# Performance work log

Measured on AMD Instinct MI355X. Metric: run time of the kernel, lower is better.

The kernel has to match this reference:

```python
import jax, jax.numpy as jnp
import numpy as np

N_NODES = 100000
N_EDGES = 200000
Z_DIM = 64
ATTR_DIM = 768
HID = 128
N_CLASSES = 5


def setup_inputs() -> dict:
    key = jax.random.key(0)
    ks = jax.random.split(key, 6)
    z = jax.random.normal(ks[0], (N_NODES, Z_DIM), dtype=jnp.float32)
    edge_index = jax.random.randint(ks[1], (2, N_EDGES), 0, N_NODES, dtype=jnp.int64)
    edge_attr = jax.random.normal(ks[2], (N_EDGES, ATTR_DIM), dtype=jnp.float32)
    W1 = jax.random.normal(ks[3], (ATTR_DIM + Z_DIM, HID), dtype=jnp.float32) * 0.02
    b1 = jnp.zeros((HID,), dtype=jnp.float32)
    W2 = jax.random.normal(ks[4], (HID, N_CLASSES), dtype=jnp.float32) * 0.02
    b2 = jnp.zeros((N_CLASSES,), dtype=jnp.float32)
    return {"z": z, "edge_index": edge_index, "edge_attr": edge_attr,
            "W1": W1, "b1": b1, "W2": W2, "b2": b2}


def reference(z, edge_index, edge_attr, W1, b1, W2, b2):
    # decode(): gather endpoint embeddings, elementwise product  [E, 64]
    node_rep = z[edge_index[0]] * z[edge_index[1]]
    # concat with edge attributes -> [E, 64 + 768] (torch cat order: node_rep first)
    joint = jnp.concatenate([node_rep, edge_attr], axis=-1)
    # 2-layer MLP + softmax
    h = jax.nn.relu(joint @ W1 + b1)
    logits = h @ W2 + b2
    return jax.nn.softmax(logits, axis=-1)
```

## Files before the change

kernel.cpp:

```cpp
#include <hip/hip_runtime.h>
#include <hip/hip_bf16.h>

#define E_TOT 200000
#define NZ 64
#define ATTR_D 768
#define HID_D 128
#define NCLS 5

typedef __attribute__((ext_vector_type(8))) short short8;
typedef __attribute__((ext_vector_type(4))) float f32x4;

typedef __attribute__((address_space(3))) unsigned       lds_u32_t;
typedef const __attribute__((address_space(1))) unsigned glob_u32_t;

__device__ __forceinline__ unsigned pk2(float a, float b) {
    __hip_bfloat162 h = __float22bfloat162_rn(make_float2(a, b));
    return *reinterpret_cast<unsigned*>(&h);
}

__device__ __forceinline__ short8 pack8(const float4 x0, const float4 x1) {
    union { unsigned u[4]; short8 s; } r;
    r.u[0] = pk2(x0.x, x0.y);
    r.u[1] = pk2(x0.z, x0.w);
    r.u[2] = pk2(x1.x, x1.y);
    r.u[3] = pk2(x1.z, x1.w);
    return r.s;
}

__global__ void prep_w1f(const float* __restrict__ W1, __hip_bfloat16* __restrict__ w1f) {
    int idx = blockIdx.x * 256 + threadIdx.x;
    if (idx >= 26 * 8 * 64 * 8) return;
    int j    = idx & 7;
    int lane = (idx >> 3) & 63;
    int f    = (idx >> 9) & 7;
    int kt   = idx >> 12;
    int n = f * 16 + (lane & 15);
    int k = kt * 32 + (lane >> 4) * 8 + j;
    w1f[idx] = __float2bfloat16(W1[(size_t)k * HID_D + n]);
}

__global__ __launch_bounds__(256, 2) void gcn_main(
    const float* __restrict__ z, const int* __restrict__ ei,
    const float* __restrict__ attr, const __hip_bfloat16* __restrict__ w1f,
    const float* __restrict__ b1, const float* __restrict__ W2,
    const float* __restrict__ b2, float* __restrict__ out) {

    __shared__ float As[4][4096];

    const int t    = threadIdx.x;
    const int wv   = t >> 6;
    const int lane = t & 63;
    const int g    = lane >> 4;
    const int c0   = lane & 15;
    const int e0   = blockIdx.x * 128;

    const float* sbase[4];
#pragma unroll
    for (int i = 0; i < 4; ++i) {
        int rsl = i * 8 + (lane >> 3);
        int cch = (lane & 7) ^ (rsl & 7);
        int er  = e0 + wv * 32 + rsl; if (er >= E_TOT) er = E_TOT - 1;
        sbase[i] = attr + (size_t)er * ATTR_D + cch * 4;
    }

#define SB __builtin_amdgcn_sched_barrier(0)
#define WAITVM(N) asm volatile("s_waitcnt vmcnt(" #N ")" ::: "memory")
#define STAGE(BUF, S)                                                          \
    {                                                                          \
        _Pragma("unroll")                                                      \
        for (int i = 0; i < 4; ++i)                                            \
            __builtin_amdgcn_global_load_lds(                                  \
                (glob_u32_t*)(sbase[i] + (S) * 32),                            \
                (lds_u32_t*)&As[BUF][wv * 1024 + i * 256],                     \
                16, 0, 0);                                                     \
    }

    const __hip_bfloat16* wf = w1f + (size_t)lane * 8;
    auto LOADB = [&](int kt, short8(&b)[8]) {
#pragma unroll
        for (int f = 0; f < 8; ++f)
            b[f] = *reinterpret_cast<const short8*>(wf + (size_t)(kt * 8 + f) * 512);
    };

    const float* zsp[2];
    const float* zdp[2];
#pragma unroll
    for (int m = 0; m < 2; ++m) {
        int e = e0 + wv * 32 + m * 16 + c0; if (e >= E_TOT) e = E_TOT - 1;
        zsp[m] = z + (size_t)ei[e] * NZ + g * 8;
        zdp[m] = z + (size_t)ei[E_TOT + e] * NZ + g * 8;
    }
    float4 zsr[2][2][2], zdr[2][2][2];
#pragma unroll
    for (int m = 0; m < 2; ++m)
#pragma unroll
        for (int kt = 0; kt < 2; ++kt)
#pragma unroll
            for (int h = 0; h < 2; ++h) {
                zsr[m][kt][h] = *reinterpret_cast<const float4*>(zsp[m] + kt * 32 + h * 4);
                zdr[m][kt][h] = *reinterpret_cast<const float4*>(zdp[m] + kt * 32 + h * 4);
            }
    SB;
    short8 bz0[8], bz1[8];
    LOADB(0, bz0); LOADB(1, bz1);
    SB;
    STAGE(0, 0); SB;
    STAGE(1, 1); SB;
    short8 bX[8], bY[8];
    LOADB(2, bX);
    SB;
    STAGE(2, 2); SB;
    LOADB(3, bY);
    SB;

    f32x4 acc[2][8];
#pragma unroll
    for (int m = 0; m < 2; ++m)
#pragma unroll
        for (int f = 0; f < 8; ++f) acc[m][f] = (f32x4){0.f, 0.f, 0.f, 0.f};

#pragma unroll
    for (int kt = 0; kt < 2; ++kt) {
        short8 a[2];
#pragma unroll
        for (int m = 0; m < 2; ++m) {
            float4 x0, x1;
            x0.x = zsr[m][kt][0].x * zdr[m][kt][0].x;
            x0.y = zsr[m][kt][0].y * zdr[m][kt][0].y;
            x0.z = zsr[m][kt][0].z * zdr[m][kt][0].z;
            x0.w = zsr[m][kt][0].w * zdr[m][kt][0].w;
            x1.x = zsr[m][kt][1].x * zdr[m][kt][1].x;
            x1.y = zsr[m][kt][1].y * zdr[m][kt][1].y;
            x1.z = zsr[m][kt][1].z * zdr[m][kt][1].z;
            x1.w = zsr[m][kt][1].w * zdr[m][kt][1].w;
            a[m] = pack8(x0, x1);
        }
#pragma unroll
        for (int f = 0; f < 8; ++f) {
            short8 bb = kt ? bz1[f] : bz0[f];
            acc[0][f] = __builtin_amdgcn_mfma_f32_16x16x32_bf16(a[0], bb, acc[0][f], 0, 0, 0);
            acc[1][f] = __builtin_amdgcn_mfma_f32_16x16x32_bf16(a[1], bb, acc[1][f], 0, 0, 0);
        }
    }

#define ITER_BODY(S, BC)                                                       \
        const float* sl = &As[(S) & 3][wv * 1024];                             \
        int pA = (2 * g) ^ (c0 & 7);                                           \
        int pB = pA ^ 1;                                                       \
        float4 x00 = *reinterpret_cast<const float4*>(sl + c0 * 32 + pA * 4);  \
        float4 x01 = *reinterpret_cast<const float4*>(sl + c0 * 32 + pB * 4);  \
        float4 x10 = *reinterpret_cast<const float4*>(sl + (c0 + 16) * 32 + pA * 4); \
        float4 x11 = *reinterpret_cast<const float4*>(sl + (c0 + 16) * 32 + pB * 4); \
        short8 a0 = pack8(x00, x01);                                           \
        short8 a1 = pack8(x10, x11);                                           \
        _Pragma("unroll")                                                      \
        for (int f = 0; f < 8; ++f) {                                          \
            acc[0][f] = __builtin_amdgcn_mfma_f32_16x16x32_bf16(a0, (BC)[f], acc[0][f], 0, 0, 0); \
            acc[1][f] = __builtin_amdgcn_mfma_f32_16x16x32_bf16(a1, (BC)[f], acc[1][f], 0, 0, 0); \
        }

#define ITER_FULL(S, BC)                                                       \
    {                                                                          \
        WAITVM(12); SB;                                                        \
        STAGE(((S) + 3) & 3, (S) + 3); SB;                                     \
        ITER_BODY(S, BC)                                                       \
        SB; LOADB((S) + 4, BC); SB;                                            \
    }
#define ITER_NOS(S, BC)                                                        \
    {                                                                          \
        WAITVM(12); SB;                                                        \
        ITER_BODY(S, BC)                                                       \
        SB; LOADB((S) + 4, BC); SB;                                            \
    }
#define ITER_BARE(S, W, BC)                                                    \
    {                                                                          \
        WAITVM(W); SB;                                                         \
        ITER_BODY(S, BC)                                                       \
    }

    ITER_FULL(0,  bX) ITER_FULL(1,  bY) ITER_FULL(2,  bX) ITER_FULL(3,  bY)
    ITER_FULL(4,  bX) ITER_FULL(5,  bY) ITER_FULL(6,  bX) ITER_FULL(7,  bY)
    ITER_FULL(8,  bX) ITER_FULL(9,  bY) ITER_FULL(10, bX) ITER_FULL(11, bY)
    ITER_FULL(12, bX) ITER_FULL(13, bY) ITER_FULL(14, bX) ITER_FULL(15, bY)
    ITER_FULL(16, bX) ITER_FULL(17, bY) ITER_FULL(18, bX) ITER_FULL(19, bY)
    ITER_FULL(20, bX)
    ITER_NOS(21, bY)
    ITER_BARE(22, 8, bX)
    ITER_BARE(23, 0, bY)
#undef ITER_FULL
#undef ITER_NOS
#undef ITER_BARE
#undef ITER_BODY
#undef STAGE
#undef WAITVM
#undef SB

    float b1v[8], w2v[8][NCLS];
#pragma unroll
    for (int f = 0; f < 8; ++f) {
        int col = f * 16 + c0;
        b1v[f] = b1[col];
#pragma unroll
        for (int cc = 0; cc < NCLS; ++cc) w2v[f][cc] = W2[col * NCLS + cc];
    }
    float b2v[NCLS];
#pragma unroll
    for (int cc = 0; cc < NCLS; ++cc) b2v[cc] = b2[cc];

#pragma unroll
    for (int m = 0; m < 2; ++m) {
#pragma unroll
        for (int i = 0; i < 4; ++i) {
            float lg[NCLS] = {0.f, 0.f, 0.f, 0.f, 0.f};
#pragma unroll
            for (int f = 0; f < 8; ++f) {
                float h = acc[m][f][i] + b1v[f];
                h = fmaxf(h, 0.f);
#pragma unroll
                for (int cc = 0; cc < NCLS; ++cc) lg[cc] = fmaf(h, w2v[f][cc], lg[cc]);
            }
#pragma unroll
            for (int mask = 1; mask < 16; mask <<= 1) {
#pragma unroll
                for (int cc = 0; cc < NCLS; ++cc) lg[cc] += __shfl_xor(lg[cc], mask);
            }
#pragma unroll
            for (int cc = 0; cc < NCLS; ++cc) lg[cc] += b2v[cc];

            float mx = fmaxf(fmaxf(fmaxf(lg[0], lg[1]), fmaxf(lg[2], lg[3])), lg[4]);
            float q[NCLS];
            float s = 0.f;
#pragma unroll
            for (int cc = 0; cc < NCLS; ++cc) { q[cc] = __expf(lg[cc] - mx); s += q[cc]; }
            float inv = 1.0f / s;
            float num = (c0 == 0) ? q[0] : (c0 == 1) ? q[1] : (c0 == 2) ? q[2]
                      : (c0 == 3) ? q[3] : q[4];
            int eo = e0 + wv * 32 + m * 16 + g * 4 + i;
            if (eo < E_TOT && c0 < NCLS) out[(size_t)eo * NCLS + c0] = num * inv;
        }
    }
}

extern "C" void kernel_launch(void* const* d_in, const int* in_sizes, int n_in,
                              void* d_out, int out_size, void* d_ws, size_t ws_size,
                              hipStream_t stream) {
    const float* z    = (const float*)d_in[0];
    const int*   ei   = (const int*)d_in[1];
    const float* attr = (const float*)d_in[2];
    const float* W1   = (const float*)d_in[3];
    const float* b1   = (const float*)d_in[4];
    const float* W2   = (const float*)d_in[5];
    const float* b2   = (const float*)d_in[6];
    float* out = (float*)d_out;
    __hip_bfloat16* w1f = (__hip_bfloat16*)d_ws;

    prep_w1f<<<(26 * 8 * 64 * 8 + 255) / 256, 256, 0, stream>>>(W1, w1f);
    const int nblk = (E_TOT + 127) / 128;
    gcn_main<<<nblk, 256, 0, stream>>>(z, ei, attr, w1f, b1, W2, b2, out);
}
```

Before: 183.1 us.

## Shrink LDS ring to three stages and compute z-term early for higher occupancy

Cuts the LDS staging ring for edge_attr tiles from four buffers to three and raises launch bounds from 2 to 3 blocks per SU. This lowers LDS use per block so more blocks can be resident. The node-embedding gather and product are restructured so z rows and W1 fragments are loaded and consumed per k-tile, which frees registers that were held across the prologue. Prefetch depth drops from three stages to two, and the vmcnt wait counts are retuned to match, so memory latency is less hidden per wave in exchange for more waves.

```diff
diff --git a/kernel.cpp b/kernel.cpp
--- a/kernel.cpp
+++ b/kernel.cpp
@@ -39,13 +39,13 @@
     w1f[idx] = __float2bfloat16(W1[(size_t)k * HID_D + n]);
 }
 
-__global__ __launch_bounds__(256, 2) void gcn_main(
+__global__ __launch_bounds__(256, 3) void gcn_main(
     const float* __restrict__ z, const int* __restrict__ ei,
     const float* __restrict__ attr, const __hip_bfloat16* __restrict__ w1f,
     const float* __restrict__ b1, const float* __restrict__ W2,
     const float* __restrict__ b2, float* __restrict__ out) {
 
-    __shared__ float As[4][4096];
+    __shared__ float As[3][4096];
 
     const int t    = threadIdx.x;
     const int wv   = t >> 6;
@@ -82,69 +82,56 @@
             b[f] = *reinterpret_cast<const short8*>(wf + (size_t)(kt * 8 + f) * 512);
     };
 
-    const float* zsp[2];
-    const float* zdp[2];
-#pragma unroll
-    for (int m = 0; m < 2; ++m) {
-        int e = e0 + wv * 32 + m * 16 + c0; if (e >= E_TOT) e = E_TOT - 1;
-        zsp[m] = z + (size_t)ei[e] * NZ + g * 8;
-        zdp[m] = z + (size_t)ei[E_TOT + e] * NZ + g * 8;
-    }
-    float4 zsr[2][2][2], zdr[2][2][2];
-#pragma unroll
-    for (int m = 0; m < 2; ++m)
-#pragma unroll
-        for (int kt = 0; kt < 2; ++kt)
-#pragma unroll
-            for (int h = 0; h < 2; ++h) {
-                zsr[m][kt][h] = *reinterpret_cast<const float4*>(zsp[m] + kt * 32 + h * 4);
-                zdr[m][kt][h] = *reinterpret_cast<const float4*>(zdp[m] + kt * 32 + h * 4);
-            }
-    SB;
-    short8 bz0[8], bz1[8];
-    LOADB(0, bz0); LOADB(1, bz1);
-    SB;
     STAGE(0, 0); SB;
     STAGE(1, 1); SB;
+
+    f32x4 acc[2][8];
+#pragma unroll
+    for (int m = 0; m < 2; ++m)
+#pragma unroll
+        for (int f = 0; f < 8; ++f) acc[m][f] = (f32x4){0.f, 0.f, 0.f, 0.f};
+
+    {
+        const float* zsp[2];
+        const float* zdp[2];
+#pragma unroll
+        for (int m = 0; m < 2; ++m) {
+            int e = e0 + wv * 32 + m * 16 + c0; if (e >= E_TOT) e = E_TOT - 1;
+            zsp[m] = z + (size_t)ei[e] * NZ + g * 8;
+            zdp[m] = z + (size_t)ei[E_TOT + e] * NZ + g * 8;
+        }
+        short8 bzz[8];
+#pragma unroll
+        for (int kt = 0; kt < 2; ++kt) {
+            LOADB(kt, bzz);
+            short8 a[2];
+#pragma unroll
+            for (int m = 0; m < 2; ++m) {
+                float4 s0 = *reinterpret_cast<const float4*>(zsp[m] + kt * 32);
+                float4 s1 = *reinterpret_cast<const float4*>(zsp[m] + kt * 32 + 4);
+                float4 d0 = *reinterpret_cast<const float4*>(zdp[m] + kt * 32);
+                float4 d1 = *reinterpret_cast<const float4*>(zdp[m] + kt * 32 + 4);
+                float4 x0, x1;
+                x0.x = s0.x * d0.x; x0.y = s0.y * d0.y; x0.z = s0.z * d0.z; x0.w = s0.w * d0.w;
+                x1.x = s1.x * d1.x; x1.y = s1.y * d1.y; x1.z = s1.z * d1.z; x1.w = s1.w * d1.w;
+                a[m] = pack8(x0, x1);
+            }
+#pragma unroll
+            for (int f = 0; f < 8; ++f) {
+                acc[0][f] = __builtin_amdgcn_mfma_f32_16x16x32_bf16(a[0], bzz[f], acc[0][f], 0, 0, 0);
+                acc[1][f] = __builtin_amdgcn_mfma_f32_16x16x32_bf16(a[1], bzz[f], acc[1][f], 0, 0, 0);
+            }
+        }
+    }
+
     short8 bX[8], bY[8];
+    SB;
     LOADB(2, bX);
-    SB;
-    STAGE(2, 2); SB;
     LOADB(3, bY);
     SB;
 
-    f32x4 acc[2][8];
-#pragma unroll
-    for (int m = 0; m < 2; ++m)
-#pragma unroll
-        for (int f = 0; f < 8; ++f) acc[m][f] = (f32x4){0.f, 0.f, 0.f, 0.f};
-
-#pragma unroll
-    for (int kt = 0; kt < 2; ++kt) {
-        short8 a[2];
-#pragma unroll
-        for (int m = 0; m < 2; ++m) {
-            float4 x0, x1;
-            x0.x = zsr[m][kt][0].x * zdr[m][kt][0].x;
-            x0.y = zsr[m][kt][0].y * zdr[m][kt][0].y;
-            x0.z = zsr[m][kt][0].z * zdr[m][kt][0].z;
-            x0.w = zsr[m][kt][0].w * zdr[m][kt][0].w;
-            x1.x = zsr[m][kt][1].x * zdr[m][kt][1].x;
-            x1.y = zsr[m][kt][1].y * zdr[m][kt][1].y;
-            x1.z = zsr[m][kt][1].z * zdr[m][kt][1].z;
-            x1.w = zsr[m][kt][1].w * zdr[m][kt][1].w;
-            a[m] = pack8(x0, x1);
-        }
-#pragma unroll
-        for (int f = 0; f < 8; ++f) {
-            short8 bb = kt ? bz1[f] : bz0[f];
-            acc[0][f] = __builtin_amdgcn_mfma_f32_16x16x32_bf16(a[0], bb, acc[0][f], 0, 0, 0);
-            acc[1][f] = __builtin_amdgcn_mfma_f32_16x16x32_bf16(a[1], bb, acc[1][f], 0, 0, 0);
-        }
-    }
-
 #define ITER_BODY(S, BC)                                                       \
-        const float* sl = &As[(S) & 3][wv * 1024];                             \
+        const float* sl = &As[(S) % 3][wv * 1024];                             \
         int pA = (2 * g) ^ (c0 & 7);                                           \
         int pB = pA ^ 1;                                                       \
         float4 x00 = *reinterpret_cast<const float4*>(sl + c0 * 32 + pA * 4);  \
@@ -159,16 +146,10 @@
             acc[1][f] = __builtin_amdgcn_mfma_f32_16x16x32_bf16(a1, (BC)[f], acc[1][f], 0, 0, 0); \
         }
 
-#define ITER_FULL(S, BC)                                                       \
+#define ITER_FULL(S, W, BC)                                                    \
     {                                                                          \
-        WAITVM(12); SB;                                                        \
-        STAGE(((S) + 3) & 3, (S) + 3); SB;                                     \
-        ITER_BODY(S, BC)                                                       \
-        SB; LOADB((S) + 4, BC); SB;                                            \
-    }
-#define ITER_NOS(S, BC)                                                        \
-    {                                                                          \
-        WAITVM(12); SB;                                                        \
+        WAITVM(W); SB;                                                         \
+        STAGE(((S) + 2) % 3, (S) + 2); SB;                                     \
         ITER_BODY(S, BC)                                                       \
         SB; LOADB((S) + 4, BC); SB;                                            \
     }
@@ -178,17 +159,17 @@
         ITER_BODY(S, BC)                                                       \
     }
 
-    ITER_FULL(0,  bX) ITER_FULL(1,  bY) ITER_FULL(2,  bX) ITER_FULL(3,  bY)
-    ITER_FULL(4,  bX) ITER_FULL(5,  bY) ITER_FULL(6,  bX) ITER_FULL(7,  bY)
-    ITER_FULL(8,  bX) ITER_FULL(9,  bY) ITER_FULL(10, bX) ITER_FULL(11, bY)
-    ITER_FULL(12, bX) ITER_FULL(13, bY) ITER_FULL(14, bX) ITER_FULL(15, bY)
-    ITER_FULL(16, bX) ITER_FULL(17, bY) ITER_FULL(18, bX) ITER_FULL(19, bY)
-    ITER_FULL(20, bX)
-    ITER_NOS(21, bY)
-    ITER_BARE(22, 8, bX)
-    ITER_BARE(23, 0, bY)
+    ITER_FULL(0,  8,  bX) ITER_FULL(1,  12, bY) ITER_FULL(2,  12, bX)
+    ITER_FULL(3,  12, bY) ITER_FULL(4,  12, bX) ITER_FULL(5,  12, bY)
+    ITER_FULL(6,  12, bX) ITER_FULL(7,  12, bY) ITER_FULL(8,  12, bX)
+    ITER_FULL(9,  12, bY) ITER_FULL(10, 12, bX) ITER_FULL(11, 12, bY)
+    ITER_FULL(12, 12, bX) ITER_FULL(13, 12, bY) ITER_FULL(14, 12, bX)
+    ITER_FULL(15, 12, bY) ITER_FULL(16, 12, bX) ITER_FULL(17, 12, bY)
+    ITER_FULL(18, 12, bX) ITER_FULL(19, 12, bY) ITER_FULL(20, 12, bX)
+    ITER_FULL(21, 12, bY)
+    ITER_BARE(22, 12, bX)
+    ITER_BARE(23, 0,  bY)
 #undef ITER_FULL
-#undef ITER_NOS
 #undef ITER_BARE
 #undef ITER_BODY
 #undef STAGE
```

After: 200.0 us. 9.2% more time.
